# Kernel tuning notes

Hardware: AMD Instinct MI355X
Metric: run time of the kernel (lower is better)

## Reference

```python
import jax, jax.numpy as jnp
import numpy as np
from jax import lax

B, C, Dd, Hh, Ww = 2, 256, 8, 64, 64
E, HID, TOPK = 6, 1024, 3


def setup_inputs() -> dict:
    key = jax.random.key(0)
    ks = jax.random.split(key, 8)
    return {
        "x": jax.random.normal(ks[0], (B, C, Dd, Hh, Ww), jnp.float32),
        "attention_weights": jax.random.uniform(ks[1], (B, Dd, Hh, Ww), jnp.float32),
        "gate_w": jax.random.normal(ks[2], (E, C), jnp.float32) * 0.02,
        "gate_b": jnp.zeros((E,), jnp.float32),
        "w1": jax.random.normal(ks[3], (E, HID, C), jnp.float32) * (1.0 / np.sqrt(C)),
        "b1": jnp.zeros((E, HID), jnp.float32),
        "w2": jax.random.normal(ks[4], (E, C, HID), jnp.float32) * (1.0 / np.sqrt(HID)),
        "b2": jnp.zeros((E, C), jnp.float32),
    }


def reference(x, attention_weights, gate_w, gate_b, w1, b1, w2, b2):
    b, c, d, h, w = x.shape
    n = d * h * w
    e = gate_w.shape[0]
    xt = x.reshape(b, c, n).transpose(0, 2, 1)  # [B, N, C] tokens
    # 1x1x1 gate conv == per-voxel linear
    gv = jnp.einsum('bnc,ec->bne', xt, gate_w) + gate_b  # [B, N, E]
    gv = gv * attention_weights.reshape(b, n, 1)
    gv = jax.nn.softmax(gv, axis=-1)  # softmax over experts (dim=1 in torch layout)
    top_v, top_i = lax.top_k(gv, TOPK)  # [B, N, 3]
    # scatter top-k softmax values into a zero mask (non-topk experts get 0)
    mask = jnp.sum(jax.nn.one_hot(top_i, e, dtype=gv.dtype) * top_v[..., None], axis=-2)  # [B, N, E]
    out = jnp.zeros_like(xt)
    for ei in range(e):  # loop over small fixed expert count
        hdn = jax.nn.gelu(jnp.einsum('bnc,hc->bnh', xt, w1[ei]) + b1[ei], approximate=False)
        o = jnp.einsum('bnh,ch->bnc', hdn, w2[ei]) + b2[ei]
        out = out + mask[:, :, ei:ei + 1] * o
    return out.transpose(0, 2, 1).reshape(b, c, d, h, w)
```

## Files before the change

kernel.cpp:

```cpp
#include <hip/hip_runtime.h>
#include <hip/hip_bf16.h>
#include <math.h>

#define NN 32768
#define CC 256
#define EE 6
#define HID 1024
#define TT 64
#define NTOK 65536
#define NTILE_MAX 1044
#define NT3MAX 3078
#define NCH 16
#define SENT 0xFFFFFFFFu

typedef __attribute__((ext_vector_type(8))) short bf16x8;
typedef __attribute__((ext_vector_type(4))) float f32x4;
typedef __attribute__((ext_vector_type(2))) float f32x2;
typedef __attribute__((ext_vector_type(4))) unsigned int u32x4;
typedef __attribute__((ext_vector_type(2))) unsigned int u32x2;

__device__ const int CMB[20][3] = {
  {0,1,2},{0,1,3},{0,1,4},{0,1,5},{0,2,3},{0,2,4},{0,2,5},{0,3,4},{0,3,5},{0,4,5},
  {1,2,3},{1,2,4},{1,2,5},{1,3,4},{1,3,5},{1,4,5},{2,3,4},{2,3,5},{2,4,5},{3,4,5}};
__device__ const unsigned char M2B[64] = {
  255,255,255,255,255,255,255,  0,
  255,255,255,  1,255,  4, 10,255,
  255,255,255,  2,255,  5, 11,255,
  255,  7, 13,255, 16,255,255,255,
  255,255,255,  3,255,  6, 12,255,
  255,  8, 14,255, 17,255,255,255,
  255,  9, 15,255, 18,255,255,255,
   19,255,255,255,255,255,255,255};

__device__ __forceinline__ unsigned short f32_bf16(float f) {
  unsigned u = __builtin_bit_cast(unsigned, f);
  u += 0x7FFFu + ((u >> 16) & 1u);
  return (unsigned short)(u >> 16);
}

__device__ __forceinline__ unsigned cvt_pk_bf16(float lo, float hi) {
  unsigned r;
  asm("v_cvt_pk_bf16_f32 %0, %1, %2" : "=v"(r) : "v"(lo), "v"(hi));
  return r;
}

__device__ __forceinline__ float fast_gelu(float v) {
  float s = v * v;
  float a = v * -2.3021181819f;
  float m = a * 0.044715f;
  float nu = __builtin_fmaf(m, s, a);
  float z = __builtin_amdgcn_exp2f(nu);
  return v * __builtin_amdgcn_rcpf(1.0f + z);
}

typedef __attribute__((address_space(3))) void lds_void;
typedef __attribute__((address_space(1))) const void glb_void;
__device__ __forceinline__ void gload16(const void* g, void* l) {
  __builtin_amdgcn_global_load_lds((glb_void*)g, (lds_void*)l, 16, 0, 0);
}

__global__ void wconv(const float* __restrict__ w1, const float* __restrict__ w2,
                      unsigned short* __restrict__ w1b, unsigned short* __restrict__ w2b) {
  int i = blockIdx.x * 256 + threadIdx.x;
  w1b[i] = f32_bf16(w1[i]);
  w2b[i] = f32_bf16(w2[i]);
}


__global__ __launch_bounds__(256) void gatepack_k(
    const float* __restrict__ x, const float* __restrict__ attn,
    const float* __restrict__ gate_w, const float* __restrict__ gate_b,
    unsigned* __restrict__ setid, float* __restrict__ wsel,
    unsigned* __restrict__ ehist, unsigned char* __restrict__ Xp3) {
  __shared__ float gws[EE * CC];
  __shared__ unsigned char lx[TT * 512];
  __shared__ float gred[256 * EE];
  __shared__ unsigned hist6[EE];

  const int tid = threadIdx.x, lane = tid & 63, wv = tid >> 6;
  const int n0g = blockIdx.x * TT;
  const int bI = n0g >> 15, n0 = n0g & (NN - 1);

  for (int i = tid; i < EE * CC; i += 256) gws[i] = gate_w[i];
  if (tid < EE) hist6[tid] = 0;
  __syncthreads();

  {
    float gp[EE] = {0.f, 0.f, 0.f, 0.f, 0.f, 0.f};
    const size_t xbase = ((size_t)bI * CC + wv * 64) * NN + n0 + lane;
    #pragma unroll 1
    for (int c8 = 0; c8 < 8; ++c8) {
      float xv[8];
      #pragma unroll
      for (int j = 0; j < 8; ++j)
        xv[j] = x[xbase + (size_t)(c8 * 8 + j) * NN];
      #pragma unroll
      for (int j = 0; j < 8; ++j) {
        int c = wv * 64 + c8 * 8 + j;
        #pragma unroll
        for (int e = 0; e < EE; ++e) gp[e] = __builtin_fmaf(xv[j], gws[e * CC + c], gp[e]);
      }
      u32x4 pk;
      #pragma unroll
      for (int q = 0; q < 4; ++q) pk[q] = cvt_pk_bf16(xv[2 * q], xv[2 * q + 1]);
      *(u32x4*)(lx + lane * 512 + (wv * 64 + c8 * 8) * 2) = pk;
    }
    #pragma unroll
    for (int e = 0; e < EE; ++e) gred[(wv * 64 + lane) * EE + e] = gp[e];
  }
  __syncthreads();

  if (tid < 64) {
    float g[EE];
    #pragma unroll
    for (int e = 0; e < EE; ++e)
      g[e] = gred[(0 * 64 + tid) * EE + e] + gred[(1 * 64 + tid) * EE + e] +
             gred[(2 * 64 + tid) * EE + e] + gred[(3 * 64 + tid) * EE + e];
    float aw = attn[n0g + tid];
    float m = -1e30f;
    #pragma unroll
    for (int e = 0; e < EE; ++e) { g[e] = (g[e] + gate_b[e]) * aw; m = fmaxf(m, g[e]); }
    float ex[EE], s = 0.f;
    #pragma unroll
    for (int e = 0; e < EE; ++e) { ex[e] = expf(g[e] - m); s += ex[e]; }
    int i1 = 0; float v1 = g[0];
    #pragma unroll
    for (int e = 1; e < EE; ++e) if (g[e] > v1) { v1 = g[e]; i1 = e; }
    int i2 = -1; float v2 = -3.4e38f;
    #pragma unroll
    for (int e = 0; e < EE; ++e) if (e != i1 && g[e] > v2) { v2 = g[e]; i2 = e; }
    int i3 = -1; float v3 = -3.4e38f;
    #pragma unroll
    for (int e = 0; e < EE; ++e) if (e != i1 && e != i2 && g[e] > v3) { v3 = g[e]; i3 = e; }
    const unsigned msk = (1u << i1) | (1u << i2) | (1u << i3);
    float inv = 1.f / s;
    int slot = 0;
    #pragma unroll
    for (int e = 0; e < EE; ++e)
      if ((msk >> e) & 1u) wsel[(size_t)(n0g + tid) * 3 + (slot++)] = ex[e] * inv;
    setid[n0g + tid] = (unsigned)M2B[msk];
    atomicAdd(&hist6[i1], 1u); atomicAdd(&hist6[i2], 1u); atomicAdd(&hist6[i3], 1u);
  }
  __syncthreads();

  #pragma unroll 1
  for (int r = 0; r < 16; ++r) {
    const int t = wv * 16 + r;
    u32x2 v = *(const u32x2*)(lx + t * 512 + lane * 8);
    *(u32x2*)(Xp3 + (size_t)(n0g + t) * 512 + lane * 8) = v;
  }
  if (tid < EE) ehist[tid * 1024 + blockIdx.x] = hist6[tid];
}

__global__ __launch_bounds__(256) void prefix3_k(
    const unsigned* __restrict__ ehist, unsigned* __restrict__ ebase,
    unsigned* __restrict__ desc3, unsigned* __restrict__ tlist3,
    float* __restrict__ wp3) {
  __shared__ unsigned sc[256];
  __shared__ unsigned tot[EE], bb[EE + 1], tcum[EE + 1];
  const int tid = threadIdx.x;
  #pragma unroll 1
  for (int e = 0; e < EE; ++e) {
    unsigned v[4]; unsigned s = 0;
    #pragma unroll
    for (int k = 0; k < 4; ++k) { v[k] = ehist[e * 1024 + tid * 4 + k]; s += v[k]; }
    sc[tid] = s; __syncthreads();
    for (int off = 1; off < 256; off <<= 1) {
      unsigned tv = (tid >= off) ? sc[tid - off] : 0u; __syncthreads();
      sc[tid] += tv; __syncthreads();
    }
    unsigned excl = sc[tid] - s;
    if (tid == 255) tot[e] = sc[255];
    unsigned run = excl;
    #pragma unroll
    for (int k = 0; k < 4; ++k) { ebase[e * 1024 + tid * 4 + k] = run; run += v[k]; }
    __syncthreads();
  }
  if (tid == 0) {
    unsigned base = 0, tc = 0;
    for (int e = 0; e < EE; ++e) {
      bb[e] = base; tcum[e] = tc;
      unsigned tl = (tot[e] + 63) >> 6;
      tc += tl; base += tl << 6;
    }
    bb[EE] = base; tcum[EE] = tc;
  }
  __syncthreads();
  #pragma unroll 1
  for (int e = 0; e < EE; ++e) {
    unsigned b0 = bb[e];
    #pragma unroll
    for (int k = 0; k < 4; ++k) ebase[e * 1024 + tid * 4 + k] += b0;
  }
  if (tid < EE) {
    for (unsigned i = bb[tid] + tot[tid]; i < bb[tid + 1]; ++i) {
      tlist3[i] = SENT; wp3[i] = 0.f;
    }
  }
  __syncthreads();
  const unsigned nt = tcum[EE];
  for (int i = tid; i < NT3MAX; i += 256) {
    unsigned d;
    if ((unsigned)i < nt) {
      int e = 0;
      while (!((unsigned)i >= tcum[e] && (unsigned)i < tcum[e + 1])) ++e;
      d = ((unsigned)e << 16) | ((bb[e] >> 6) + ((unsigned)i - tcum[e]));
    } else d = 0x003F0000u;
    desc3[i] = d;
  }
}

__global__ __launch_bounds__(64) void scatter3_k(
    const unsigned* __restrict__ setid, const unsigned* __restrict__ ebase,
    const float* __restrict__ wsel,
    unsigned* __restrict__ tlist3, float* __restrict__ wp3, unsigned* __restrict__ pos3) {
  const int tid = threadIdx.x;
  const int blk = blockIdx.x;
  const unsigned id = blk * 64 + tid;
  const unsigned bkt = setid[id];
  const unsigned m6 =
      (1u << CMB[bkt][0]) | (1u << CMB[bkt][1]) | (1u << CMB[bkt][2]);
  const unsigned long long below = (1ull << tid) - 1ull;
  int s = 0;
  #pragma unroll
  for (int e = 0; e < EE; ++e) {
    unsigned long long bl = __ballot((m6 >> e) & 1u);
    if ((m6 >> e) & 1u) {
      unsigned rank = (unsigned)__builtin_popcountll(bl & below);
      unsigned p = ebase[e * 1024 + blk] + rank;
      tlist3[p] = id;
      wp3[p] = wsel[(size_t)id * 3 + s];
      pos3[(size_t)id * 3 + s] = p;
      s++;
    }
  }
}

__global__ __launch_bounds__(512, 2) void moe_main3(
    const float* __restrict__ b1, const float* __restrict__ b2,
    const unsigned short* __restrict__ w1b, const unsigned short* __restrict__ w2b,
    const unsigned* __restrict__ desc3, const unsigned* __restrict__ tlist3,
    const float* __restrict__ wp3, const unsigned char* __restrict__ Xp3,
    unsigned char* __restrict__ Op3) {
  __shared__ unsigned char lds[143872];
  unsigned char* hs = lds + 131072;
  float* b1S = (float*)(lds + 139264);
  unsigned* tokS = (unsigned*)(lds + 143360);
  float* w3S = (float*)(lds + 143616);

  const unsigned d = desc3[blockIdx.x];
  const unsigned e = d >> 16;
  if (e > 5) return;
  const int lstart = (int)(d & 0xFFFFu) << 6;

  const int tid  = threadIdx.x;
  const int lane = tid & 63;
  const int wv   = tid >> 6;
  const int lr   = lane & 15;
  const int lg   = lane >> 4;
  const int wt   = wv >> 2;
  const int wh   = wv & 3;

  if (tid < TT) { tokS[tid] = tlist3[lstart + tid]; w3S[tid] = wp3[lstart + tid]; }
  *(f32x2*)&b1S[tid * 2] = *(const f32x2*)&b1[e * HID + tid * 2];
  __syncthreads();

  const unsigned char* w1bytes = (const unsigned char*)w1b + (size_t)e * HID * 512;
  const unsigned char* w2bytes = (const unsigned char*)w2b + (size_t)e * CC * 2048;

  auto STAGE = [&](int bufsel, int k2) {
    unsigned char* wb = lds + bufsel * 65536;
    #pragma unroll
    for (int i = 0; i < 4; ++i) {
      unsigned slot = (unsigned)(wv * 4096 + i * 1024 + lane * 16);
      unsigned h = slot >> 9;
      unsigned off = (slot & 511u) ^ ((h & 7u) << 4);
      gload16(w1bytes + ((size_t)(k2 * 64 + h) << 9) + off, wb + slot);
    }
    #pragma unroll
    for (int i = 0; i < 4; ++i) {
      unsigned slot = (unsigned)(wv * 4096 + i * 1024 + lane * 16);
      unsigned c = slot >> 7;
      unsigned off = (slot & 127u) ^ ((c & 7u) << 4);
      gload16(w2bytes + (size_t)c * 2048 + (unsigned)(k2 * 128) + off,
              wb + 32768 + slot);
    }
  };

  STAGE(0, 0);
  STAGE(1, 1);
  asm volatile("" ::: "memory");

  bf16x8 bx[2][8];
  #pragma unroll
  for (int fnl = 0; fnl < 2; ++fnl) {
    int t = wt * 32 + fnl * 16 + lr;
    unsigned tk = tokS[t];
    if (tk == SENT) tk = 0u;
    const unsigned char* xr = Xp3 + (size_t)tk * 512;
    #pragma unroll
    for (int ks = 0; ks < 8; ++ks)
      bx[fnl][ks] = *(const bf16x8*)(xr + ks * 64 + lg * 16);
  }
  asm volatile("s_waitcnt vmcnt(24)" ::: "memory");
  __builtin_amdgcn_s_barrier();
  asm volatile("" ::: "memory");

  f32x4 oacc[2][4];
  #pragma unroll
  for (int cf = 0; cf < 2; ++cf)
    #pragma unroll
    for (int fn = 0; fn < 4; ++fn) oacc[cf][fn] = (f32x4){0.f, 0.f, 0.f, 0.f};

  const unsigned myrow = (unsigned)(wh * 16 + lr);
  const unsigned rsw   = (myrow & 7u) << 4;

  #pragma unroll 1
  for (int k = 0; k < NCH; ++k) {
    unsigned char* wb = lds + (k & 1) * 65536;

    f32x4 hacc[2];
    hacc[0] = (f32x4){0.f, 0.f, 0.f, 0.f};
    hacc[1] = (f32x4){0.f, 0.f, 0.f, 0.f};
    __builtin_amdgcn_s_setprio(1);
    #pragma unroll
    for (int ks = 0; ks < 8; ++ks) {
      bf16x8 af = *(const bf16x8*)(wb + myrow * 512 +
                                   (((unsigned)(ks * 64 + lg * 16)) ^ rsw));
      hacc[0] = __builtin_amdgcn_mfma_f32_16x16x32_bf16(af, bx[0][ks], hacc[0], 0, 0, 0);
      hacc[1] = __builtin_amdgcn_mfma_f32_16x16x32_bf16(af, bx[1][ks], hacc[1], 0, 0, 0);
    }
    __builtin_amdgcn_s_setprio(0);

    {
      f32x4 b1v = *(const f32x4*)&b1S[k * 64 + wh * 16 + lg * 4];
      #pragma unroll
      for (int fnl = 0; fnl < 2; ++fnl) {
        int t = wt * 32 + fnl * 16 + lr;
        float msk = w3S[t];
        float gg[4];
        #pragma unroll
        for (int r = 0; r < 4; ++r)
          gg[r] = fast_gelu(hacc[fnl][r] + b1v[r]) * msk;
        u32x2 pk;
        pk[0] = cvt_pk_bf16(gg[0], gg[1]);
        pk[1] = cvt_pk_bf16(gg[2], gg[3]);
        *(u32x2*)(hs + t * 128 +
                  (((unsigned)(wh * 32 + lg * 8)) ^ (((unsigned)(t & 7)) << 4))) = pk;
      }
    }
    asm volatile("s_waitcnt lgkmcnt(0)" ::: "memory");
    __builtin_amdgcn_s_barrier();
    asm volatile("" ::: "memory");

    __builtin_amdgcn_s_setprio(1);
    #pragma unroll
    for (int ks2 = 0; ks2 < 2; ++ks2) {
      bf16x8 bh[4];
      #pragma unroll
      for (int fn = 0; fn < 4; ++fn) {
        int t = fn * 16 + lr;
        bh[fn] = *(const bf16x8*)(hs + t * 128 +
                  (((unsigned)(ks2 * 64 + lg * 16)) ^ (((unsigned)(t & 7)) << 4)));
      }
      #pragma unroll
      for (int cf = 0; cf < 2; ++cf) {
        unsigned c = (unsigned)(wv * 32 + cf * 16 + lr);
        bf16x8 am = *(const bf16x8*)(wb + 32768 + c * 128 +
                    (((unsigned)(ks2 * 64 + lg * 16)) ^ ((c & 7u) << 4)));
        #pragma unroll
        for (int fn = 0; fn < 4; ++fn)
          oacc[cf][fn] =
              __builtin_amdgcn_mfma_f32_16x16x32_bf16(am, bh[fn], oacc[cf][fn], 0, 0, 0);
      }
    }
    __builtin_amdgcn_s_setprio(0);

    if (k < NCH - 1) {
      asm volatile("" ::: "memory");
      __builtin_amdgcn_s_barrier();
      asm volatile("" ::: "memory");
      if (k + 2 < NCH) {
        STAGE(k & 1, k + 2);
        asm volatile("s_waitcnt vmcnt(8)" ::: "memory");
      } else {
        asm volatile("s_waitcnt vmcnt(0)" ::: "memory");
      }
      __builtin_amdgcn_s_barrier();
      asm volatile("" ::: "memory");
    }
  }

  float wt3[4];
  #pragma unroll
  for (int fn = 0; fn < 4; ++fn) wt3[fn] = w3S[fn * 16 + lr];
  #pragma unroll
  for (int cf = 0; cf < 2; ++cf) {
    f32x4 b2v = *(const f32x4*)&b2[e * CC + wv * 32 + cf * 16 + lg * 4];
    #pragma unroll
    for (int fn = 0; fn < 4; ++fn)
      #pragma unroll
      for (int r = 0; r < 4; ++r)
        oacc[cf][fn][r] = __builtin_fmaf(wt3[fn], b2v[r], oacc[cf][fn][r]);
  }
  #pragma unroll
  for (int fn = 0; fn < 4; ++fn) {
    const int row = lstart + fn * 16 + lr;
    unsigned char* po = Op3 + (size_t)row * 512;
    #pragma unroll
    for (int cf = 0; cf < 2; ++cf) {
      u32x2 pk;
      pk[0] = cvt_pk_bf16(oacc[cf][fn][0], oacc[cf][fn][1]);
      pk[1] = cvt_pk_bf16(oacc[cf][fn][2], oacc[cf][fn][3]);
      *(u32x2*)(po + (wv * 32 + cf * 16 + lg * 4) * 2) = pk;
    }
  }
}

__global__ __launch_bounds__(256) void unscatter3_k(
    const unsigned char* __restrict__ Op3, const unsigned* __restrict__ pos3,
    float* __restrict__ out) {
  __shared__ float lo[32 * 261];
  __shared__ unsigned psf[96];
  const int tid = threadIdx.x;
  const int n0g = blockIdx.x * 32;
  const int b = n0g >> 15, n0 = n0g & (NN - 1);

  if (tid < 96) psf[tid] = pos3[(size_t)n0g * 3 + tid];
  __syncthreads();

  #pragma unroll
  for (int j = 0; j < 8; ++j) {
    const int row = j * 4 + (tid >> 6);
    const int c = (tid & 63) * 4;
    float a0 = 0.f, a1 = 0.f, a2 = 0.f, a3 = 0.f;
    #pragma unroll
    for (int s = 0; s < 3; ++s) {
      const unsigned r = psf[row * 3 + s];
      u32x2 v = *(const u32x2*)(Op3 + (size_t)r * 512 + c * 2);
      a0 += __builtin_bit_cast(float, v[0] << 16);
      a1 += __builtin_bit_cast(float, v[0] & 0xFFFF0000u);
      a2 += __builtin_bit_cast(float, v[1] << 16);
      a3 += __builtin_bit_cast(float, v[1] & 0xFFFF0000u);
    }
    lo[row * 261 + c + 0] = a0; lo[row * 261 + c + 1] = a1;
    lo[row * 261 + c + 2] = a2; lo[row * 261 + c + 3] = a3;
  }
  __syncthreads();

  const int noff = tid & 31, cq = tid >> 5;
  float* po = out + (size_t)b * CC * NN + n0 + noff;
  #pragma unroll
  for (int j2 = 0; j2 < 32; ++j2) {
    int c = cq * 32 + j2;
    po[(size_t)c * NN] = lo[noff * 261 + c];
  }
}


__global__ __launch_bounds__(256) void gate_k(
    const float* __restrict__ x, const float* __restrict__ attn,
    const float* __restrict__ gate_w, const float* __restrict__ gate_b,
    unsigned* __restrict__ setid, float* __restrict__ wsel,
    unsigned* __restrict__ bhist) {
  __shared__ float gws[EE * CC];
  __shared__ unsigned hist[20];
  const int tid = threadIdx.x;
  const int blk = blockIdx.x;
  for (int i = tid; i < EE * CC; i += 256) gws[i] = gate_w[i];
  if (tid < 20) hist[tid] = 0;
  __syncthreads();

  const unsigned id = blk * 256 + tid;
  const int b = id >> 15, n = id & (NN - 1);
  const float* px = x + (size_t)b * CC * NN + n;
  float g[EE] = {0.f, 0.f, 0.f, 0.f, 0.f, 0.f};
  #pragma unroll 4
  for (int c = 0; c < CC; ++c) {
    float xv = px[(size_t)c * NN];
    #pragma unroll
    for (int e = 0; e < EE; ++e) g[e] = __builtin_fmaf(xv, gws[e * CC + c], g[e]);
  }
  float aw = attn[id];
  float m = -1e30f;
  #pragma unroll
  for (int e = 0; e < EE; ++e) { g[e] = (g[e] + gate_b[e]) * aw; m = fmaxf(m, g[e]); }
  float ex[EE], s = 0.f;
  #pragma unroll
  for (int e = 0; e < EE; ++e) { ex[e] = expf(g[e] - m); s += ex[e]; }
  int i1 = 0; float v1 = g[0];
  #pragma unroll
  for (int e = 1; e < EE; ++e) if (g[e] > v1) { v1 = g[e]; i1 = e; }
  int i2 = -1; float v2 = -3.4e38f;
  #pragma unroll
  for (int e = 0; e < EE; ++e) if (e != i1 && g[e] > v2) { v2 = g[e]; i2 = e; }
  int i3 = -1; float v3 = -3.4e38f;
  #pragma unroll
  for (int e = 0; e < EE; ++e) if (e != i1 && e != i2 && g[e] > v3) { v3 = g[e]; i3 = e; }
  const unsigned msk = (1u << i1) | (1u << i2) | (1u << i3);
  const unsigned bkt = M2B[msk];
  float inv = 1.f / s;
  int slot = 0;
  #pragma unroll
  for (int e = 0; e < EE; ++e)
    if ((msk >> e) & 1u) wsel[(size_t)id * 3 + (slot++)] = ex[e] * inv;
  setid[id] = bkt;
  atomicAdd(&hist[bkt], 1u);
  __syncthreads();
  if (tid < 20) bhist[blk * 20 + tid] = hist[tid];
}

__global__ void prefix_k(const unsigned* __restrict__ bhist, unsigned* __restrict__ bbase,
                         unsigned* __restrict__ desc) {
  __shared__ unsigned tot[20];
  __shared__ unsigned bb[21];
  __shared__ unsigned tcum[21];
  const int tid = threadIdx.x;
  if (tid < 20) {
    unsigned run = 0;
    for (int blk = 0; blk < 256; ++blk) {
      unsigned v = bhist[blk * 20 + tid];
      bbase[blk * 20 + tid] = run;
      run += v;
    }
    tot[tid] = run;
  }
  __syncthreads();
  if (tid == 0) {
    unsigned base = 0, tc = 0;
    for (int b = 0; b < 20; ++b) {
      bb[b] = base; tcum[b] = tc;
      unsigned tl = (tot[b] + 63) >> 6;
      tc += tl; base += tl << 6;
    }
    bb[20] = base; tcum[20] = tc;
  }
  __syncthreads();
  if (tid < 20) {
    unsigned b0 = bb[tid];
    for (int blk = 0; blk < 256; ++blk) bbase[blk * 20 + tid] += b0;
  }
  __syncthreads();
  const unsigned nt = tcum[20];
  for (int i = tid; i < NTILE_MAX; i += 256) {
    unsigned d;
    if ((unsigned)i < nt) {
      int b = 0;
      while (!((unsigned)i >= tcum[b] && (unsigned)i < tcum[b + 1])) ++b;
      d = ((unsigned)b << 16) | ((bb[b] >> 6) + ((unsigned)i - tcum[b]));
    } else {
      d = 0x003F0000u;
    }
    desc[i] = d;
  }
}

__global__ __launch_bounds__(256) void scatter_k(
    const unsigned* __restrict__ setid, const unsigned* __restrict__ bbase,
    const float* __restrict__ wsel,
    unsigned* __restrict__ pos, float* __restrict__ wp) {
  __shared__ unsigned wcnt[4][20];
  const int tid = threadIdx.x, lane = tid & 63, w = tid >> 6;
  const int blk = blockIdx.x;
  const unsigned id = blk * 256 + tid;
  const unsigned sid = setid[id];
  unsigned long long myb = 0;
  #pragma unroll
  for (int b = 0; b < 20; ++b) {
    unsigned long long bl = __ballot(sid == (unsigned)b);
    if (lane == 0) wcnt[w][b] = (unsigned)__builtin_popcountll(bl);
    if ((unsigned)b == sid) myb = bl;
  }
  __syncthreads();
  unsigned rank = 0;
  #pragma unroll
  for (int w2 = 0; w2 < 4; ++w2) if (w2 < w) rank += wcnt[w2][sid];
  rank += (unsigned)__builtin_popcountll(myb & ((1ull << lane) - 1ull));
  const unsigned p = bbase[blk * 20 + sid] + rank;
  pos[id] = p;
  #pragma unroll
  for (int s = 0; s < 3; ++s) wp[(size_t)p * 3 + s] = wsel[(size_t)id * 3 + s];
}

__global__ __launch_bounds__(256) void xpack_k(
    const float* __restrict__ x, const unsigned* __restrict__ pos,
    unsigned char* __restrict__ Xp) {
  __shared__ unsigned char lx[TT * 512];
  __shared__ unsigned posS[TT];
  const int tid = threadIdx.x, lane = tid & 63, wv = tid >> 6;
  const int n0g = blockIdx.x * TT;
  const int b = n0g >> 15, n0 = n0g & (NN - 1);

  if (tid < TT) posS[tid] = pos[n0g + tid];

  const float* px = x + (size_t)b * CC * NN + n0 + lane;
  #pragma unroll 1
  for (int c8 = 0; c8 < 8; ++c8) {
    float xv[8];
    #pragma unroll
    for (int j = 0; j < 8; ++j)
      xv[j] = px[(size_t)(wv * 64 + c8 * 8 + j) * NN];
    u32x4 pk;
    #pragma unroll
    for (int q = 0; q < 4; ++q) pk[q] = cvt_pk_bf16(xv[2 * q], xv[2 * q + 1]);
    *(u32x4*)(lx + lane * 512 + (wv * 64 + c8 * 8) * 2) = pk;
  }
  __syncthreads();

  #pragma unroll 1
  for (int r = 0; r < 16; ++r) {
    const int t = wv * 16 + r;
    const unsigned p = posS[t];
    u32x2 v = *(const u32x2*)(lx + t * 512 + lane * 8);
    *(u32x2*)(Xp + (size_t)p * 512 + (((unsigned)(lane * 8)) ^ (((unsigned)(p & 31)) << 4))) = v;
  }
}

__global__ __launch_bounds__(256, 2) void moe_main(
    const float* __restrict__ b1, const float* __restrict__ b2,
    const unsigned short* __restrict__ w1b, const unsigned short* __restrict__ w2b,
    const unsigned* __restrict__ desc, const float* __restrict__ wp,
    const unsigned char* __restrict__ Xp, float* __restrict__ Op) {
  __shared__ unsigned char xs[TT * CC * 2];
  __shared__ unsigned char hs[TT * 256 * 2];
  __shared__ float w3S[3 * TT];

  const unsigned d = desc[blockIdx.x];
  const unsigned bkt = d >> 16;
  if (bkt > 19) return;
  const int lstart = (int)(d & 0xFFFFu) << 6;

  const int tid  = threadIdx.x;
  const int lane = tid & 63;
  const int wv   = tid >> 6;
  const int lr   = lane & 15;
  const int lg   = lane >> 4;

  if (tid < 3 * TT) {
    int t = tid & 63, s = tid >> 6;
    w3S[s * 64 + t] = wp[(size_t)(lstart + t) * 3 + s];
  }

  {
    const unsigned char* src = Xp + (size_t)lstart * 512;
    #pragma unroll
    for (int it = 0; it < 8; ++it) {
      u32x4 v = *(const u32x4*)(src + it * 4096 + tid * 16);
      *(u32x4*)(xs + it * 4096 + tid * 16) = v;
    }
  }
  __syncthreads();

  f32x4 oacc[4][4];
  #pragma unroll
  for (int fm = 0; fm < 4; ++fm)
    #pragma unroll
    for (int fn = 0; fn < 4; ++fn) oacc[fm][fn] = (f32x4){0.f, 0.f, 0.f, 0.f};

  unsigned trowA[4], tswA[4];
  #pragma unroll
  for (int fn = 0; fn < 4; ++fn) {
    int t = fn * 16 + lr;
    trowA[fn] = (unsigned)t * 512u;
    tswA[fn]  = ((unsigned)(t & 31)) << 4;
  }

  #pragma unroll 1
  for (int xe = 0; xe < 3; ++xe) {
    const int e = CMB[bkt][xe];
    #pragma unroll 1
    for (int sc = 0; sc < 4; ++sc) {
      f32x4 hacc[4][4];
      #pragma unroll
      for (int fm = 0; fm < 4; ++fm)
        #pragma unroll
        for (int fn = 0; fn < 4; ++fn) hacc[fm][fn] = (f32x4){0.f, 0.f, 0.f, 0.f};
      const unsigned short* w1p =
          w1b + ((size_t)(e * HID + sc * 256 + wv * 64 + lr)) * CC + lg * 8;
      #pragma unroll
      for (int ks = 0; ks < 8; ++ks) {
        bf16x8 af[4], bxv[4];
        #pragma unroll
        for (int fm = 0; fm < 4; ++fm)
          af[fm] = *(const bf16x8*)(w1p + fm * 16 * CC + ks * 32);
        #pragma unroll
        for (int fn = 0; fn < 4; ++fn)
          bxv[fn] = *(const bf16x8*)(xs + trowA[fn] +
                                    (((unsigned)(ks * 64 + lg * 16)) ^ tswA[fn]));
        #pragma unroll
        for (int fn = 0; fn < 4; ++fn)
          #pragma unroll
          for (int fm = 0; fm < 4; ++fm)
            hacc[fm][fn] =
                __builtin_amdgcn_mfma_f32_16x16x32_bf16(af[fm], bxv[fn], hacc[fm][fn], 0, 0, 0);
      }
      {
        f32x4 b1v[4];
        #pragma unroll
        for (int fm = 0; fm < 4; ++fm)
          b1v[fm] = *(const f32x4*)&b1[e * HID + sc * 256 + wv * 64 + fm * 16 + lg * 4];
        #pragma unroll
        for (int fn = 0; fn < 4; ++fn) {
          float msk = w3S[xe * 64 + fn * 16 + lr];
          #pragma unroll
          for (int fm = 0; fm < 4; ++fm) {
            float gg[4];
            #pragma unroll
            for (int r = 0; r < 4; ++r)
              gg[r] = fast_gelu(hacc[fm][fn][r] + b1v[fm][r]) * msk;
            u32x2 pk;
            pk[0] = cvt_pk_bf16(gg[0], gg[1]);
            pk[1] = cvt_pk_bf16(gg[2], gg[3]);
            unsigned byteo = trowA[fn] +
                (((unsigned)((wv * 64 + fm * 16 + lg * 4) * 2)) ^ tswA[fn]);
            *(u32x2*)(hs + byteo) = pk;
          }
        }
      }
      __syncthreads();
      const unsigned short* w2p =
          w2b + ((size_t)(e * CC + wv * 64 + lr)) * HID + sc * 256 + lg * 8;
      #pragma unroll
      for (int ks = 0; ks < 8; ++ks) {
        bf16x8 am[4], bh[4];
        #pragma unroll
        for (int fm = 0; fm < 4; ++fm)
          am[fm] = *(const bf16x8*)(w2p + fm * 16 * HID + ks * 32);
        #pragma unroll
        for (int fn = 0; fn < 4; ++fn)
          bh[fn] = *(const bf16x8*)(hs + trowA[fn] +
                                    (((unsigned)(ks * 64 + lg * 16)) ^ tswA[fn]));
        #pragma unroll
        for (int fn = 0; fn < 4; ++fn)
          #pragma unroll
          for (int fm = 0; fm < 4; ++fm)
            oacc[fm][fn] =
                __builtin_amdgcn_mfma_f32_16x16x32_bf16(am[fm], bh[fn], oacc[fm][fn], 0, 0, 0);
      }
      __syncthreads();
    }
  }

  #pragma unroll
  for (int xe = 0; xe < 3; ++xe) {
    const int e = CMB[bkt][xe];
    float msk[4];
    #pragma unroll
    for (int fn = 0; fn < 4; ++fn) msk[fn] = w3S[xe * 64 + fn * 16 + lr];
    #pragma unroll
    for (int fm = 0; fm < 4; ++fm) {
      f32x4 b2v = *(const f32x4*)&b2[e * CC + wv * 64 + fm * 16 + lg * 4];
      #pragma unroll
      for (int fn = 0; fn < 4; ++fn)
        #pragma unroll
        for (int r = 0; r < 4; ++r)
          oacc[fm][fn][r] = __builtin_fmaf(msk[fn], b2v[r], oacc[fm][fn][r]);
    }
  }
  #pragma unroll
  for (int fn = 0; fn < 4; ++fn) {
    float* po = Op + (size_t)(lstart + fn * 16 + lr) * CC;
    #pragma unroll
    for (int fm = 0; fm < 4; ++fm)
      *(f32x4*)(po + wv * 64 + fm * 16 + lg * 4) = oacc[fm][fn];
  }
}

__global__ __launch_bounds__(256) void unscatter_k(
    const float* __restrict__ Op, const unsigned* __restrict__ pos,
    float* __restrict__ out) {
  __shared__ float lo[32 * 261];
  __shared__ unsigned posS[32];
  const int tid = threadIdx.x;
  const int n0g = blockIdx.x * 32;
  const int b = n0g >> 15, n0 = n0g & (NN - 1);

  if (tid < 32) posS[tid] = pos[n0g + tid];
  __syncthreads();

  #pragma unroll
  for (int j = 0; j < 8; ++j) {
    int fidx = j * 1024 + tid * 4;
    int row = fidx >> 8, c = fidx & 255;
    f32x4 v = *(const f32x4*)(Op + (size_t)posS[row] * CC + c);
    #pragma unroll
    for (int i = 0; i < 4; ++i) lo[row * 261 + c + i] = v[i];
  }
  __syncthreads();

  const int noff = tid & 31, cq = tid >> 5;
  float* po = out + (size_t)b * CC * NN + n0 + noff;
  #pragma unroll
  for (int j2 = 0; j2 < 32; ++j2) {
    int c = cq * 32 + j2;
    po[(size_t)c * NN] = lo[noff * 261 + c];
  }
}


extern "C" void kernel_launch(void* const* d_in, const int* in_sizes, int n_in,
                              void* d_out, int out_size, void* d_ws, size_t ws_size,
                              hipStream_t stream) {
  const float* x      = (const float*)d_in[0];
  const float* attn   = (const float*)d_in[1];
  const float* gate_w = (const float*)d_in[2];
  const float* gate_b = (const float*)d_in[3];
  const float* w1     = (const float*)d_in[4];
  const float* b1     = (const float*)d_in[5];
  const float* w2     = (const float*)d_in[6];
  const float* b2     = (const float*)d_in[7];
  float* out = (float*)d_out;

  unsigned char* ws = (unsigned char*)d_ws;
  unsigned short* w1b  = (unsigned short*)(ws);
  unsigned short* w2b  = (unsigned short*)(ws + 3145728);
  unsigned*       setid= (unsigned*)(ws + 6291456);
  float*          wsel = (float*)(ws + 6553600);
  unsigned*       bhist= (unsigned*)(ws + 7340032);
  unsigned*       bbase= (unsigned*)(ws + 7360512);
  unsigned*       desc = (unsigned*)(ws + 7381120);
  unsigned*       pos  = (unsigned*)(ws + 7385344);
  float*          wp   = (float*)(ws + 7647488);
  unsigned char*  Xp   = (unsigned char*)(ws + 8449280);
  float*          Op   = (float*)(ws + 42659072);
  const size_t need_bucket = 111078656;
  unsigned*       ehist = (unsigned*)(ws + 7360512);
  unsigned*       ebase = (unsigned*)(ws + 7385088);
  unsigned*       desc3 = (unsigned*)(ws + 7409664);
  unsigned*       tlist3= (unsigned*)(ws + 7436288);
  float*          wp3   = (float*)(ws + 8224256);
  unsigned*       pos3  = (unsigned*)(ws + 9012224);
  unsigned char*  Xp3   = (unsigned char*)(ws + 9798656);
  unsigned char*  Op3   = (unsigned char*)(ws + 43353088);
  const size_t need3 = 144212992;

  wconv<<<(EE * HID * CC) / 256, 256, 0, stream>>>(w1, w2, w1b, w2b);
  if (ws_size >= need3) {
    gatepack_k<<<NTOK / TT, 256, 0, stream>>>(x, attn, gate_w, gate_b, setid, wsel, ehist, Xp3);
    prefix3_k<<<1, 256, 0, stream>>>(ehist, ebase, desc3, tlist3, wp3);
    scatter3_k<<<NTOK / 64, 64, 0, stream>>>(setid, ebase, wsel, tlist3, wp3, pos3);
    moe_main3<<<NT3MAX, 512, 0, stream>>>(b1, b2, w1b, w2b, desc3, tlist3, wp3, Xp3, Op3);
    unscatter3_k<<<NTOK / 32, 256, 0, stream>>>(Op3, pos3, out);
  } else {
    gate_k<<<NTOK / 256, 256, 0, stream>>>(x, attn, gate_w, gate_b, setid, wsel, bhist);
    prefix_k<<<1, 256, 0, stream>>>(bhist, bbase, desc);
    scatter_k<<<NTOK / 256, 256, 0, stream>>>(setid, bbase, wsel, pos, wp);
    xpack_k<<<NTOK / TT, 256, 0, stream>>>(x, pos, Xp);
    moe_main<<<NTILE_MAX, 256, 0, stream>>>(b1, b2, w1b, w2b, desc, wp, Xp, Op);
    unscatter_k<<<NTOK / 32, 256, 0, stream>>>(Op, pos, out);
  }
}
```

Baseline: 500.1 us.

## Halve hidden chunk and LDS footprint to double occupancy, split weight staging

The hidden dimension is now processed in 32-wide chunks instead of 64, which roughly halves the LDS buffers so the launch bound can allow four blocks per CU instead of two. Each wave now owns one 16-token group instead of two, and the XOR swizzle is replaced by a k-major weight layout plus a padded row stride for the hidden tile. The w1 prefetch for chunk k+2 is issued right after the first barrier, separately from the w2 prefetch, to overlap it with the second GEMM. In exchange the loop runs twice as many iterations with more barriers, and each operand read from LDS feeds fewer MFMAs.

```diff
diff --git a/kernel.cpp b/kernel.cpp
--- a/kernel.cpp
+++ b/kernel.cpp
@@ -10,7 +10,7 @@
 #define NTOK 65536
 #define NTILE_MAX 1044
 #define NT3MAX 3078
-#define NCH 16
+#define NCH 32
 #define SENT 0xFFFFFFFFu
 
 typedef __attribute__((ext_vector_type(8))) short bf16x8;
@@ -236,17 +236,17 @@
   }
 }
 
-__global__ __launch_bounds__(512, 2) void moe_main3(
+__global__ __launch_bounds__(512, 4) void moe_main3(
     const float* __restrict__ b1, const float* __restrict__ b2,
     const unsigned short* __restrict__ w1b, const unsigned short* __restrict__ w2b,
     const unsigned* __restrict__ desc3, const unsigned* __restrict__ tlist3,
     const float* __restrict__ wp3, const unsigned char* __restrict__ Xp3,
     unsigned char* __restrict__ Op3) {
-  __shared__ unsigned char lds[143872];
-  unsigned char* hs = lds + 131072;
-  float* b1S = (float*)(lds + 139264);
-  unsigned* tokS = (unsigned*)(lds + 143360);
-  float* w3S = (float*)(lds + 143616);
+  __shared__ unsigned char lds[75264];
+  unsigned char* hs = lds + 65536;
+  float* b1S = (float*)(lds + 70656);
+  unsigned* tokS = (unsigned*)(lds + 74752);
+  float* w3S = (float*)(lds + 75008);
 
   const unsigned d = desc3[blockIdx.x];
   const unsigned e = d >> 16;
@@ -258,8 +258,8 @@
   const int wv   = tid >> 6;
   const int lr   = lane & 15;
   const int lg   = lane >> 4;
-  const int wt   = wv >> 2;
-  const int wh   = wv & 3;
+  const int wt   = wv & 3;
+  const int wh   = wv >> 2;
 
   if (tid < TT) { tokS[tid] = tlist3[lstart + tid]; w3S[tid] = wp3[lstart + tid]; }
   *(f32x2*)&b1S[tid * 2] = *(const f32x2*)&b1[e * HID + tid * 2];
@@ -268,41 +268,41 @@
   const unsigned char* w1bytes = (const unsigned char*)w1b + (size_t)e * HID * 512;
   const unsigned char* w2bytes = (const unsigned char*)w2b + (size_t)e * CC * 2048;
 
-  auto STAGE = [&](int bufsel, int k2) {
-    unsigned char* wb = lds + bufsel * 65536;
-    #pragma unroll
-    for (int i = 0; i < 4; ++i) {
-      unsigned slot = (unsigned)(wv * 4096 + i * 1024 + lane * 16);
-      unsigned h = slot >> 9;
-      unsigned off = (slot & 511u) ^ ((h & 7u) << 4);
-      gload16(w1bytes + ((size_t)(k2 * 64 + h) << 9) + off, wb + slot);
-    }
-    #pragma unroll
-    for (int i = 0; i < 4; ++i) {
-      unsigned slot = (unsigned)(wv * 4096 + i * 1024 + lane * 16);
-      unsigned c = slot >> 7;
-      unsigned off = (slot & 127u) ^ ((c & 7u) << 4);
-      gload16(w2bytes + (size_t)c * 2048 + (unsigned)(k2 * 128) + off,
-              wb + 32768 + slot);
+  auto STAGE1 = [&](int bufsel, int k2) {
+    unsigned char* wb = lds + bufsel * 32768;
+    #pragma unroll
+    for (int i = 0; i < 2; ++i) {
+      unsigned s = (unsigned)(wv * 2048 + i * 1024 + lane * 16);
+      unsigned kb = s >> 9, h = (s & 511u) >> 4;
+      gload16(w1bytes + ((size_t)(k2 * 32 + h) << 9) + kb * 16, wb + s);
     }
   };
-
-  STAGE(0, 0);
-  STAGE(1, 1);
+  auto STAGE2 = [&](int bufsel, int k2) {
+    unsigned char* wb = lds + bufsel * 32768 + 16384;
+    #pragma unroll
+    for (int i = 0; i < 2; ++i) {
+      unsigned s = (unsigned)(wv * 2048 + i * 1024 + lane * 16);
+      unsigned kb = s >> 12, c = (s & 4095u) >> 4;
+      gload16(w2bytes + (size_t)c * 2048 + (unsigned)(k2 * 64) + kb * 16, wb + s);
+    }
+  };
+
+  STAGE1(0, 0); STAGE2(0, 0);
+  STAGE1(1, 1); STAGE2(1, 1);
   asm volatile("" ::: "memory");
 
-  bf16x8 bx[2][8];
-  #pragma unroll
-  for (int fnl = 0; fnl < 2; ++fnl) {
-    int t = wt * 32 + fnl * 16 + lr;
-    unsigned tk = tokS[t];
+  const int myt = wt * 16 + lr;
+  const float mskT = w3S[myt];
+  bf16x8 bx[8];
+  {
+    unsigned tk = tokS[myt];
     if (tk == SENT) tk = 0u;
     const unsigned char* xr = Xp3 + (size_t)tk * 512;
     #pragma unroll
     for (int ks = 0; ks < 8; ++ks)
-      bx[fnl][ks] = *(const bf16x8*)(xr + ks * 64 + lg * 16);
-  }
-  asm volatile("s_waitcnt vmcnt(24)" ::: "memory");
+      bx[ks] = *(const bf16x8*)(xr + ks * 64 + lg * 16);
+  }
+  asm volatile("s_waitcnt vmcnt(8)" ::: "memory");
   __builtin_amdgcn_s_barrier();
   asm volatile("" ::: "memory");
 
@@ -312,62 +312,47 @@
     #pragma unroll
     for (int fn = 0; fn < 4; ++fn) oacc[cf][fn] = (f32x4){0.f, 0.f, 0.f, 0.f};
 
-  const unsigned myrow = (unsigned)(wh * 16 + lr);
-  const unsigned rsw   = (myrow & 7u) << 4;
+  const unsigned myh16 = (unsigned)((wh * 16 + lr) * 16);
 
   #pragma unroll 1
   for (int k = 0; k < NCH; ++k) {
-    unsigned char* wb = lds + (k & 1) * 65536;
-
-    f32x4 hacc[2];
-    hacc[0] = (f32x4){0.f, 0.f, 0.f, 0.f};
-    hacc[1] = (f32x4){0.f, 0.f, 0.f, 0.f};
+    unsigned char* wb = lds + (k & 1) * 32768;
+
+    f32x4 hacc = (f32x4){0.f, 0.f, 0.f, 0.f};
     __builtin_amdgcn_s_setprio(1);
     #pragma unroll
     for (int ks = 0; ks < 8; ++ks) {
-      bf16x8 af = *(const bf16x8*)(wb + myrow * 512 +
-                                   (((unsigned)(ks * 64 + lg * 16)) ^ rsw));
-      hacc[0] = __builtin_amdgcn_mfma_f32_16x16x32_bf16(af, bx[0][ks], hacc[0], 0, 0, 0);
-      hacc[1] = __builtin_amdgcn_mfma_f32_16x16x32_bf16(af, bx[1][ks], hacc[1], 0, 0, 0);
+      bf16x8 af = *(const bf16x8*)(wb + (unsigned)((ks * 4 + lg) * 512) + myh16);
+      hacc = __builtin_amdgcn_mfma_f32_16x16x32_bf16(af, bx[ks], hacc, 0, 0, 0);
     }
     __builtin_amdgcn_s_setprio(0);
 
     {
-      f32x4 b1v = *(const f32x4*)&b1S[k * 64 + wh * 16 + lg * 4];
-      #pragma unroll
-      for (int fnl = 0; fnl < 2; ++fnl) {
-        int t = wt * 32 + fnl * 16 + lr;
-        float msk = w3S[t];
-        float gg[4];
-        #pragma unroll
-        for (int r = 0; r < 4; ++r)
-          gg[r] = fast_gelu(hacc[fnl][r] + b1v[r]) * msk;
-        u32x2 pk;
-        pk[0] = cvt_pk_bf16(gg[0], gg[1]);
-        pk[1] = cvt_pk_bf16(gg[2], gg[3]);
-        *(u32x2*)(hs + t * 128 +
-                  (((unsigned)(wh * 32 + lg * 8)) ^ (((unsigned)(t & 7)) << 4))) = pk;
-      }
+      f32x4 b1v = *(const f32x4*)&b1S[k * 32 + wh * 16 + lg * 4];
+      float gg[4];
+      #pragma unroll
+      for (int r = 0; r < 4; ++r)
+        gg[r] = fast_gelu(hacc[r] + b1v[r]) * mskT;
+      u32x2 pk;
+      pk[0] = cvt_pk_bf16(gg[0], gg[1]);
+      pk[1] = cvt_pk_bf16(gg[2], gg[3]);
+      *(u32x2*)(hs + myt * 80 + wh * 32 + lg * 8) = pk;
     }
     asm volatile("s_waitcnt lgkmcnt(0)" ::: "memory");
     __builtin_amdgcn_s_barrier();
     asm volatile("" ::: "memory");
+    if (k + 2 < NCH) STAGE1(k & 1, k + 2);
 
     __builtin_amdgcn_s_setprio(1);
-    #pragma unroll
-    for (int ks2 = 0; ks2 < 2; ++ks2) {
+    {
       bf16x8 bh[4];
       #pragma unroll
-      for (int fn = 0; fn < 4; ++fn) {
-        int t = fn * 16 + lr;
-        bh[fn] = *(const bf16x8*)(hs + t * 128 +
-                  (((unsigned)(ks2 * 64 + lg * 16)) ^ (((unsigned)(t & 7)) << 4)));
-      }
+      for (int fn = 0; fn < 4; ++fn)
+        bh[fn] = *(const bf16x8*)(hs + (fn * 16 + lr) * 80 + lg * 16);
       #pragma unroll
       for (int cf = 0; cf < 2; ++cf) {
-        unsigned c = (unsigned)(wv * 32 + cf * 16 + lr);
-        bf16x8 am = *(const bf16x8*)(wb + 32768 + c * 128 +
-                    (((unsigned)(ks2 * 64 + lg * 16)) ^ ((c & 7u) << 4)));
+        bf16x8 am = *(const bf16x8*)(wb + 16384 + lg * 4096 +
+                                     (unsigned)((wv * 32 + cf * 16 + lr) * 16));
         #pragma unroll
         for (int fn = 0; fn < 4; ++fn)
           oacc[cf][fn] =
@@ -381,8 +366,8 @@
       __builtin_amdgcn_s_barrier();
       asm volatile("" ::: "memory");
       if (k + 2 < NCH) {
-        STAGE(k & 1, k + 2);
-        asm volatile("s_waitcnt vmcnt(8)" ::: "memory");
+        STAGE2(k & 1, k + 2);
+        asm volatile("s_waitcnt vmcnt(4)" ::: "memory");
       } else {
         asm volatile("s_waitcnt vmcnt(0)" ::: "memory");
       }
```

Result: no change. 504.4 us (+0.8%).

## Split weight staging into W1/W2 phases and use chunk-major LDS layout

Applied to the files above, without the earlier changes.

Splits the per-chunk weight prefetch into two parts. The W1 tile for chunk k+2 is issued right after the hidden-activation barrier, once GEMM1 no longer reads it. The W2 tile is issued after the end-of-iteration barrier. This removes one workgroup barrier per iteration and starts W1 loads earlier. The LDS tiles move from XOR-swizzled row-major to a 16-byte-chunk-major layout, so consecutive lanes read consecutive rows without swizzle arithmetic. In exchange, the initial wait now happens before the X fragment loads are issued, which may expose more startup latency.

```diff
diff --git a/kernel.cpp b/kernel.cpp
--- a/kernel.cpp
+++ b/kernel.cpp
@@ -268,27 +268,30 @@
   const unsigned char* w1bytes = (const unsigned char*)w1b + (size_t)e * HID * 512;
   const unsigned char* w2bytes = (const unsigned char*)w2b + (size_t)e * CC * 2048;
 
-  auto STAGE = [&](int bufsel, int k2) {
+  auto STAGE1 = [&](int bufsel, int k2) {
     unsigned char* wb = lds + bufsel * 65536;
     #pragma unroll
     for (int i = 0; i < 4; ++i) {
-      unsigned slot = (unsigned)(wv * 4096 + i * 1024 + lane * 16);
-      unsigned h = slot >> 9;
-      unsigned off = (slot & 511u) ^ ((h & 7u) << 4);
-      gload16(w1bytes + ((size_t)(k2 * 64 + h) << 9) + off, wb + slot);
-    }
+      unsigned kb = (unsigned)(wv * 4 + i);
+      gload16(w1bytes + ((size_t)(k2 * 64 + lane) << 9) + kb * 16,
+              wb + kb * 1024 + lane * 16);
+    }
+  };
+  auto STAGE2 = [&](int bufsel, int k2) {
+    unsigned char* wb = lds + bufsel * 65536 + 32768;
     #pragma unroll
     for (int i = 0; i < 4; ++i) {
-      unsigned slot = (unsigned)(wv * 4096 + i * 1024 + lane * 16);
-      unsigned c = slot >> 7;
-      unsigned off = (slot & 127u) ^ ((c & 7u) << 4);
-      gload16(w2bytes + (size_t)c * 2048 + (unsigned)(k2 * 128) + off,
-              wb + 32768 + slot);
+      unsigned q = (unsigned)(wv * 4 + i);
+      unsigned kb = q >> 2, c = (q & 3u) * 64 + lane;
+      gload16(w2bytes + (size_t)c * 2048 + (unsigned)(k2 * 128) + kb * 16,
+              wb + q * 1024 + lane * 16);
     }
   };
 
-  STAGE(0, 0);
-  STAGE(1, 1);
+  STAGE1(0, 0); STAGE2(0, 0);
+  STAGE1(1, 1); STAGE2(1, 1);
+  asm volatile("s_waitcnt vmcnt(8)" ::: "memory");
+  __builtin_amdgcn_s_barrier();
   asm volatile("" ::: "memory");
 
   bf16x8 bx[2][8];
@@ -302,9 +305,6 @@
     for (int ks = 0; ks < 8; ++ks)
       bx[fnl][ks] = *(const bf16x8*)(xr + ks * 64 + lg * 16);
   }
-  asm volatile("s_waitcnt vmcnt(24)" ::: "memory");
-  __builtin_amdgcn_s_barrier();
-  asm volatile("" ::: "memory");
 
   f32x4 oacc[2][4];
   #pragma unroll
@@ -312,8 +312,7 @@
     #pragma unroll
     for (int fn = 0; fn < 4; ++fn) oacc[cf][fn] = (f32x4){0.f, 0.f, 0.f, 0.f};
 
-  const unsigned myrow = (unsigned)(wh * 16 + lr);
-  const unsigned rsw   = (myrow & 7u) << 4;
+  const unsigned myh16 = (unsigned)((wh * 16 + lr) * 16);
 
   #pragma unroll 1
   for (int k = 0; k < NCH; ++k) {
@@ -325,8 +324,7 @@
     __builtin_amdgcn_s_setprio(1);
     #pragma unroll
     for (int ks = 0; ks < 8; ++ks) {
-      bf16x8 af = *(const bf16x8*)(wb + myrow * 512 +
-                                   (((unsigned)(ks * 64 + lg * 16)) ^ rsw));
+      bf16x8 af = *(const bf16x8*)(wb + (unsigned)((ks * 4 + lg) * 1024) + myh16);
       hacc[0] = __builtin_amdgcn_mfma_f32_16x16x32_bf16(af, bx[0][ks], hacc[0], 0, 0, 0);
       hacc[1] = __builtin_amdgcn_mfma_f32_16x16x32_bf16(af, bx[1][ks], hacc[1], 0, 0, 0);
     }
@@ -352,6 +350,7 @@
     asm volatile("s_waitcnt lgkmcnt(0)" ::: "memory");
     __builtin_amdgcn_s_barrier();
     asm volatile("" ::: "memory");
+    if (k + 2 < NCH) STAGE1(k & 1, k + 2);
 
     __builtin_amdgcn_s_setprio(1);
     #pragma unroll
@@ -365,9 +364,9 @@
       }
       #pragma unroll
       for (int cf = 0; cf < 2; ++cf) {
-        unsigned c = (unsigned)(wv * 32 + cf * 16 + lr);
-        bf16x8 am = *(const bf16x8*)(wb + 32768 + c * 128 +
-                    (((unsigned)(ks2 * 64 + lg * 16)) ^ ((c & 7u) << 4)));
+        bf16x8 am = *(const bf16x8*)(wb + 32768 +
+                     (unsigned)((ks2 * 4 + lg) * 4096) +
+                     (unsigned)((wv * 32 + cf * 16 + lr) * 16));
         #pragma unroll
         for (int fn = 0; fn < 4; ++fn)
           oacc[cf][fn] =
@@ -377,17 +376,14 @@
     __builtin_amdgcn_s_setprio(0);
 
     if (k < NCH - 1) {
-      asm volatile("" ::: "memory");
-      __builtin_amdgcn_s_barrier();
-      asm volatile("" ::: "memory");
       if (k + 2 < NCH) {
-        STAGE(k & 1, k + 2);
-        asm volatile("s_waitcnt vmcnt(8)" ::: "memory");
+        asm volatile("s_waitcnt vmcnt(4)" ::: "memory");
       } else {
         asm volatile("s_waitcnt vmcnt(0)" ::: "memory");
       }
       __builtin_amdgcn_s_barrier();
       asm volatile("" ::: "memory");
+      if (k + 2 < NCH) STAGE2(k & 1, k + 2);
     }
   }
 
```

Result: slower. 576.2 us (+15.2%).
